# Performance work log

Hardware: AMD Instinct MI355X
Metric: run time of the kernel (lower is better)

## Reference

```python
import jax, jax.numpy as jnp
import numpy as np

TWO_PI = 2.0 * np.pi


def _fftfreq(n, d):
    # numpy-compatible fftfreq, trace/grad-safe in d: [0..n/2-1, -n/2..-1]/(n*d)
    k = jnp.arange(n)
    k = jnp.where(k < (n + 1) // 2, k, k - n).astype(jnp.float32)
    return k / (n * d)


def _forward(x, wp1_re, wp1_im, wp2_re, wp2_im, wr_re, wr_im, ty, tx):
    wp1 = (wp1_re + 1j * wp1_im).astype(jnp.complex64)   # [Ci,Co,m1]
    wp2 = (wp2_re + 1j * wp2_im).astype(jnp.complex64)   # [Ci,Co,m2]
    wr = (wr_re + 1j * wr_im).astype(jnp.complex64)      # [Ci,Co,m1,m2]
    Ny, Nx = x.shape[-2], x.shape[-1]
    dty = ty[1] - ty[0]
    dtx = tx[1] - tx[0]

    alpha = jnp.fft.fft2(x, axes=(-2, -1))               # [B,Ci,Ny,Nx] complex
    lam1 = (1j * TWO_PI * _fftfreq(Ny, dty)).astype(jnp.complex64)  # [Ny]
    lam2 = (1j * TWO_PI * _fftfreq(Nx, dtx)).astype(jnp.complex64)  # [Nx]

    # Pole-residue transfer function factors: Hw = wr / ((lam1-p1)(lam2-p2))
    A1 = 1.0 / (lam1 - wp1[..., None])                   # [Ci,Co,m1,Ny]
    A2 = 1.0 / (lam2 - wp2[..., None])                   # [Ci,Co,m2,Nx]

    # sum over poles (p,q) of Hw -> [Ci,Co,Ny,Nx]
    Hsum = jnp.einsum('ikpq,ikpo,ikqx->ikox', wr, A1, A2)
    res1 = jnp.einsum('biox,ikox->bkox', alpha, Hsum)    # [B,Co,Ny,Nx]
    # sum over frequency grid (o,x) -> residue coefficients [B,Co,m1,m2]
    res2 = jnp.einsum('biox,ikpq,ikpo,ikqx->bkpq', alpha, wr, A1, A2)

    x1 = jnp.real(jnp.fft.ifft2(res1, s=(Ny, Nx), axes=(-2, -1)))

    # explicit pole-exponential evaluation over the spatial grid
    E1 = jnp.exp(wp1[..., None] * ty.astype(jnp.complex64))  # [Ci,Co,m1,Ny]
    E2 = jnp.exp(wp2[..., None] * tx.astype(jnp.complex64))  # [Ci,Co,m2,Nx]
    # res2 channel dim contracts against E1/E2's first (in==out required)
    x2 = jnp.real(jnp.einsum('kbpq,bipz,biqx->kizx', res2, E1, E2)) / (Nx * Ny)
    return x1 + x2


def setup_inputs() -> dict:
    key = jax.random.key(0)
    B, Ci, Co, Ny, Nx, m1, m2 = 8, 32, 32, 128, 128, 4, 5
    ks = jax.random.split(key, 7)
    scale = 1.0 / (Ci * Co)
    x = jax.random.normal(ks[0], (B, Ci, Ny, Nx), jnp.float32)
    wp1_re = scale * jax.random.uniform(ks[1], (Ci, Co, m1), jnp.float32)
    wp1_im = scale * jax.random.uniform(ks[2], (Ci, Co, m1), jnp.float32)
    wp2_re = scale * jax.random.uniform(ks[3], (Ci, Co, m2), jnp.float32)
    wp2_im = scale * jax.random.uniform(ks[4], (Ci, Co, m2), jnp.float32)
    wr_re = scale * jax.random.uniform(ks[5], (Ci, Co, m1, m2), jnp.float32)
    wr_im = scale * jax.random.uniform(ks[6], (Ci, Co, m1, m2), jnp.float32)
    ty = (jnp.arange(Ny) / Ny).astype(jnp.float32)
    tx = (jnp.arange(Nx) / Nx).astype(jnp.float32)
    return dict(x=x, wp1_re=wp1_re, wp1_im=wp1_im, wp2_re=wp2_re, wp2_im=wp2_im,
                wr_re=wr_re, wr_im=wr_im, ty=ty, tx=tx)


def reference(x, wp1_re, wp1_im, wp2_re, wp2_im, wr_re, wr_im, ty, tx):
    return _forward(x, wp1_re, wp1_im, wp2_re, wp2_im, wr_re, wr_im, ty, tx)
```

## Files before the change

### kernel.cpp

```cpp
#include <hip/hip_runtime.h>
#include <math.h>

#define N 128
#define B 8
#define CI 32
#define CO 32
#define M1 4
#define M2 5
#define IK (CI*CO)
#define IKP (IK*M1)
#define IKQ (IK*M2)
#define TWO_PI_F 6.2831853071795864769f

__device__ __forceinline__ float2 cmul(float2 a, float2 b){
    return make_float2(fmaf(a.x,b.x,-(a.y*b.y)), fmaf(a.x,b.y,a.y*b.x));
}
__device__ __forceinline__ float2 cmadd(float2 acc, float2 a, float2 b){
    acc.x = fmaf(a.x, b.x, fmaf(-a.y, b.y, acc.x));
    acc.y = fmaf(a.x, b.y, fmaf( a.y, b.x, acc.y));
    return acc;
}

__global__ void k_A1T(const float* wr_, const float* wi_, const float* t_, float2* A1T){
    int idx = blockIdx.x*256 + threadIdx.x;
    int o   = idx >> 12;
    int ikp = idx & (IKP-1);
    float d = t_[1]-t_[0];
    float invnd = 1.0f/((float)N*d);
    int kk = (o < N/2) ? o : o - N;
    float lam = TWO_PI_F * (float)kk * invnd;
    float dr = -wr_[ikp];
    float di = lam - wi_[ikp];
    float inv = 1.0f/(dr*dr + di*di);
    A1T[idx] = make_float2(dr*inv, -di*inv);
}

__global__ void k_A2(const float* wr_, const float* wi_, const float* t_, float2* A2){
    int idx = blockIdx.x*256 + threadIdx.x;
    int ikq = idx >> 7; int xx = idx & (N-1);
    float d = t_[1]-t_[0];
    float invnd = 1.0f/((float)N*d);
    int kk = (xx < N/2) ? xx : xx - N;
    float lam = TWO_PI_F * (float)kk * invnd;
    float dr = -wr_[ikq];
    float di = lam - wi_[ikq];
    float inv = 1.0f/(dr*dr + di*di);
    A2[idx] = make_float2(dr*inv, -di*inv);
}

__global__ void k_E(const float* wr_, const float* wi_, const float* t_, float2* E){
    int idx = blockIdx.x*256 + threadIdx.x;
    int ikp = idx >> 7; int y = idx & (N-1);
    float t = t_[y];
    float m = expf(wr_[ikp]*t);
    float s, c; sincosf(wi_[ikp]*t, &s, &c);
    E[idx] = make_float2(m*c, m*s);
}

__global__ void k_W2N(const float* wrr, const float* wri, const float2* A2, float2* W2N){
    int idx = blockIdx.x*256 + threadIdx.x;
    int ikp = idx >> 7; int xx = idx & (N-1);
    int ik = ikp >> 2; int p = ikp & 3;
    float2 acc = make_float2(0.f,0.f);
    const float* wr0 = wrr + ik*(M1*M2) + p*M2;
    const float* wi0 = wri + ik*(M1*M2) + p*M2;
    const float2* a2 = A2 + (size_t)ik*(M2*N) + xx;
    #pragma unroll
    for(int q=0;q<M2;q++){
        float2 w = make_float2(wr0[q], wi0[q]);
        acc = cmadd(acc, w, a2[q*N]);
    }
    W2N[(size_t)ikp*N + xx] = acc;
}

template<int SIGNPOS, int REALIN, int SCALE>
__global__ void __launch_bounds__(256) k_fft_rows(const void* in_, float2* out){
    const float sgn = SIGNPOS ? 1.0f : -1.0f;
    __shared__ float tre[16*132];
    __shared__ float tim_[16*132];
    __shared__ float zre[16*136];
    __shared__ float zim[16*136];
    int t = threadIdx.x;
    size_t row0 = (size_t)blockIdx.x * 16;

    if(REALIN){
        const float* src = (const float*)in_ + row0*N;
        #pragma unroll
        for(int j=0;j<8;j++){
            int idx = t + 256*j; int r = idx>>7, cl = idx&127;
            tre[r*132+cl] = src[idx];
        }
    } else {
        const float2* src = (const float2*)in_ + row0*N;
        #pragma unroll
        for(int j=0;j<8;j++){
            int idx = t + 256*j; int r = idx>>7, cl = idx&127;
            float2 v = src[idx];
            tre[r*132+cl] = v.x; tim_[r*132+cl] = v.y;
        }
    }
    float t16c[16], t16s[16];
    #pragma unroll
    for(int j=0;j<16;j++){ float s,c; sincosf(sgn*(TWO_PI_F/16.f)*(float)j, &s,&c); t16c[j]=c; t16s[j]=s; }
    __syncthreads();

    int r = t>>4, u = t&15, b = u&7, h = u>>3;
    float xr[16], xi[16];
    #pragma unroll
    for(int a=0;a<16;a++){
        float vr = tre[r*132 + 8*a + b];
        float vi = REALIN ? 0.f : tim_[r*132 + 8*a + b];
        if(h && (a&1)){ vr = -vr; vi = -vi; }
        xr[a]=vr; xi[a]=vi;
    }
    #pragma unroll
    for(int cc=0; cc<8; cc++){
        float yr=0.f, yi=0.f;
        #pragma unroll
        for(int a=0;a<16;a++){
            int j = (a*cc)&15;
            if(REALIN){
                yr = fmaf(xr[a], t16c[j], yr);
                yi = fmaf(xr[a], t16s[j], yi);
            } else {
                yr = fmaf(xr[a], t16c[j], yr); yr = fmaf(-xi[a], t16s[j], yr);
                yi = fmaf(xr[a], t16s[j], yi); yi = fmaf( xi[a], t16c[j], yi);
            }
        }
        int c = 8*h + cc;
        float s,co; sincosf(sgn*(TWO_PI_F/128.f)*(float)(b*c), &s,&co);
        zre[r*136 + b*17 + c] = fmaf(yr,co,-(yi*s));
        zim[r*136 + b*17 + c] = fmaf(yr,s,  yi*co);
    }
    __syncthreads();

    float t8c[8], t8s[8];
    #pragma unroll
    for(int j=0;j<8;j++){ float s,c; sincosf(sgn*(TWO_PI_F/8.f)*(float)j, &s,&c); t8c[j]=c; t8s[j]=s; }
    int r2 = t>>4, c2 = t&15;
    float zr_[8], zi_[8];
    #pragma unroll
    for(int bb=0;bb<8;bb++){ zr_[bb]=zre[r2*136 + bb*17 + c2]; zi_[bb]=zim[r2*136 + bb*17 + c2]; }
    float2* dst = out + (row0 + r2)*N;
    #pragma unroll
    for(int d=0; d<8; d++){
        float Xr=0.f, Xi=0.f;
        #pragma unroll
        for(int bb=0;bb<8;bb++){
            int j=(bb*d)&7;
            Xr = fmaf(zr_[bb], t8c[j], Xr); Xr = fmaf(-zi_[bb], t8s[j], Xr);
            Xi = fmaf(zr_[bb], t8s[j], Xi); Xi = fmaf( zi_[bb], t8c[j], Xi);
        }
        if(SCALE){ Xr *= (1.f/128.f); Xi *= (1.f/128.f); }
        dst[c2 + 16*d] = make_float2(Xr, Xi);
    }
}

template<int SIGNPOS, int REALOUT, int SCALE>
__global__ void __launch_bounds__(256) k_fft_cols(const float2* in, float2* outc, float* outr){
    const float sgn = SIGNPOS ? 1.0f : -1.0f;
    __shared__ float tre[N*17];
    __shared__ float tim_[N*17];
    __shared__ float zre[8*16*17];
    __shared__ float zim[8*16*17];
    int t = threadIdx.x;
    int img = blockIdx.x >> 3; int x0 = (blockIdx.x & 7)*16;
    const float2* src = in + (size_t)img*N*N + x0;
    #pragma unroll
    for(int j=0;j<8;j++){
        int idx = t + 256*j; int y = idx>>4, xc = idx&15;
        float2 v = src[y*N + xc];
        tre[y*17+xc]=v.x; tim_[y*17+xc]=v.y;
    }
    float t16c[16], t16s[16];
    #pragma unroll
    for(int j=0;j<16;j++){ float s,c; sincosf(sgn*(TWO_PI_F/16.f)*(float)j, &s,&c); t16c[j]=c; t16s[j]=s; }
    __syncthreads();

    int xc = t&15, u = t>>4, b = u&7, h = u>>3;
    float xr[16], xi[16];
    #pragma unroll
    for(int a=0;a<16;a++){
        int y = 8*a + b;
        float vr = tre[y*17+xc];
        float vi = tim_[y*17+xc];
        if(h && (a&1)){ vr = -vr; vi = -vi; }
        xr[a]=vr; xi[a]=vi;
    }
    #pragma unroll
    for(int cc=0; cc<8; cc++){
        float yr=0.f, yi=0.f;
        #pragma unroll
        for(int a=0;a<16;a++){
            int j = (a*cc)&15;
            yr = fmaf(xr[a], t16c[j], yr); yr = fmaf(-xi[a], t16s[j], yr);
            yi = fmaf(xr[a], t16s[j], yi); yi = fmaf( xi[a], t16c[j], yi);
        }
        int c = 8*h + cc;
        float s,co; sincosf(sgn*(TWO_PI_F/128.f)*(float)(b*c), &s,&co);
        zre[(b*16 + c)*17 + xc] = fmaf(yr,co,-(yi*s));
        zim[(b*16 + c)*17 + xc] = fmaf(yr,s,  yi*co);
    }
    __syncthreads();

    float t8c[8], t8s[8];
    #pragma unroll
    for(int j=0;j<8;j++){ float s,c; sincosf(sgn*(TWO_PI_F/8.f)*(float)j, &s,&c); t8c[j]=c; t8s[j]=s; }
    int c2 = t>>4; int x2 = t&15;
    float zr_[8], zi_[8];
    #pragma unroll
    for(int bb=0;bb<8;bb++){ zr_[bb]=zre[(bb*16 + c2)*17 + x2]; zi_[bb]=zim[(bb*16 + c2)*17 + x2]; }
    #pragma unroll
    for(int d=0; d<8; d++){
        float Xr=0.f, Xi=0.f;
        #pragma unroll
        for(int bb=0;bb<8;bb++){
            int j=(bb*d)&7;
            Xr = fmaf(zr_[bb], t8c[j], Xr); Xr = fmaf(-zi_[bb], t8s[j], Xr);
            Xi = fmaf(zr_[bb], t8s[j], Xi); Xi = fmaf( zi_[bb], t8c[j], Xi);
        }
        int ky = c2 + 16*d;
        if(REALOUT){
            outr[(size_t)img*N*N + ky*N + x0 + x2] = Xr * (SCALE ? (1.f/128.f) : 1.f);
        } else {
            if(SCALE){ Xr *= (1.f/128.f); Xi *= (1.f/128.f); }
            outc[(size_t)img*N*N + ky*N + x0 + x2] = make_float2(Xr, Xi);
        }
    }
}

__global__ void __launch_bounds__(256) k_res1(const float2* alpha, const float2* A1T,
                                              const float2* W2N, float2* res1){
    __shared__ float4 At4[B*CI*8];
    int t = threadIdx.x;
    int o  = blockIdx.x >> 3;
    int x0 = (blockIdx.x & 7) * 16;

    {
        int im0 = t >> 3, xq = t & 7;
        #pragma unroll
        for(int j=0;j<8;j++){
            int im = im0 + 32*j;
            At4[im*8 + xq] = *(const float4*)(alpha + (size_t)im*(N*N) + o*N + x0 + 2*xq);
        }
    }
    __syncthreads();

    int k = t >> 3, xh = t & 7;
    float2 acc[B][2];
    #pragma unroll
    for(int b=0;b<B;b++){ acc[b][0]=make_float2(0.f,0.f); acc[b][1]=make_float2(0.f,0.f); }

    const float2* a1base = A1T + (size_t)o*IKP + k*M1;
    const float2* w2base = W2N + ((size_t)k*M1)*N + x0 + 2*xh;

    #pragma unroll 2
    for(int i=0;i<CI;i++){
        float4 a1a = *(const float4*)(a1base + (size_t)i*128);
        float4 a1b = *(const float4*)(a1base + (size_t)i*128 + 2);
        float2 a1v[M1] = { make_float2(a1a.x,a1a.y), make_float2(a1a.z,a1a.w),
                           make_float2(a1b.x,a1b.y), make_float2(a1b.z,a1b.w) };
        float2 h0 = make_float2(0.f,0.f), h1 = make_float2(0.f,0.f);
        const float2* w2 = w2base + (size_t)i*(128*N);
        #pragma unroll
        for(int p=0;p<M1;p++){
            float4 wv = *(const float4*)(w2 + (size_t)p*N);
            h0 = cmadd(h0, a1v[p], make_float2(wv.x,wv.y));
            h1 = cmadd(h1, a1v[p], make_float2(wv.z,wv.w));
        }
        #pragma unroll
        for(int b=0;b<B;b++){
            float4 av = At4[(b*CI + i)*8 + xh];
            acc[b][0] = cmadd(acc[b][0], make_float2(av.x,av.y), h0);
            acc[b][1] = cmadd(acc[b][1], make_float2(av.z,av.w), h1);
        }
    }

    #pragma unroll
    for(int b=0;b<B;b++){
        float4 v = make_float4(acc[b][0].x, acc[b][0].y, acc[b][1].x, acc[b][1].y);
        *(float4*)(res1 + (size_t)(b*CO + k)*(N*N) + o*N + x0 + 2*xh) = v;
    }
}

__global__ void __launch_bounds__(512, 4) k_S_res2(const float2* alpha, const float2* A2,
                                                   const float2* A1T, float2* part){
    __shared__ float2 tile[64*33];
    __shared__ float2 A2c[160*33];
    int t = threadIdx.x;
    int ol = t & 15;
    int kl = t >> 4;
    int bid = blockIdx.x;
    int oh = bid & 1;
    int i  = (bid >> 1) & (CI-1);
    int b  = bid >> 6;
    int ik = i*CO + kl;
    const float2* asrc = alpha + ((size_t)(b*CI + i))*(N*N) + (size_t)oh*64*N;
    const float2* a2base = A2 + (size_t)i*(CO*M2*N);

    const int txc = t & 31, trow = t >> 5;
    float2 U[4][5];
    #pragma unroll
    for(int oi=0;oi<4;oi++)
        #pragma unroll
        for(int q=0;q<5;q++) U[oi][q] = make_float2(0.f,0.f);

    float2 pre[4];
    #pragma unroll
    for(int j=0;j<4;j++) pre[j] = asrc[(trow + 16*j)*N + txc];

    for(int c=0; c<4; c++){
        __syncthreads();
        #pragma unroll
        for(int j=0;j<4;j++) tile[(trow + 16*j)*33 + txc] = pre[j];
        #pragma unroll
        for(int s=0;s<10;s++){
            int rs = s*16 + trow;
            A2c[rs*33 + txc] = a2base[(size_t)rs*N + c*32 + txc];
        }
        if(c < 3){
            #pragma unroll
            for(int j=0;j<4;j++) pre[j] = asrc[(trow + 16*j)*N + (c+1)*32 + txc];
        }
        __syncthreads();
        #pragma unroll 4
        for(int xc=0; xc<32; xc++){
            float2 a2v[5];
            const float2* a2row = A2c + (kl*5)*33 + xc;
            #pragma unroll
            for(int q=0;q<5;q++) a2v[q] = a2row[q*33];
            #pragma unroll
            for(int oi=0;oi<4;oi++){
                float2 av = tile[(ol + 16*oi)*33 + xc];
                #pragma unroll
                for(int q=0;q<5;q++) U[oi][q] = cmadd(U[oi][q], av, a2v[q]);
            }
        }
    }

    float2 S[4][5];
    #pragma unroll
    for(int p=0;p<4;p++)
        #pragma unroll
        for(int q=0;q<5;q++) S[p][q] = make_float2(0.f,0.f);
    #pragma unroll
    for(int oi=0;oi<4;oi++){
        int o = oh*64 + ol + 16*oi;
        const float2* a1 = A1T + (size_t)o*IKP + (size_t)ik*M1;
        float2 a1v[4];
        #pragma unroll
        for(int p=0;p<4;p++) a1v[p] = a1[p];
        #pragma unroll
        for(int p=0;p<4;p++)
            #pragma unroll
            for(int q=0;q<5;q++) S[p][q] = cmadd(S[p][q], a1v[p], U[oi][q]);
    }
    #pragma unroll
    for(int m=1;m<16;m<<=1){
        #pragma unroll
        for(int p=0;p<4;p++)
            #pragma unroll
            for(int q=0;q<5;q++){
                S[p][q].x += __shfl_xor(S[p][q].x, m);
                S[p][q].y += __shfl_xor(S[p][q].y, m);
            }
    }
    if(ol==0){
        float2* dst = part + ((size_t)((b*CO + kl)*CI + i)*2 + oh)*(M1*M2);
        #pragma unroll
        for(int p=0;p<4;p++)
            #pragma unroll
            for(int q=0;q<5;q++) dst[p*5+q] = S[p][q];
    }
}

__global__ void k_res2_red(const float2* part, const float* wrr, const float* wri, float2* res2){
    int bk = blockIdx.x;
    int t = threadIdx.x;
    int i = t & 31, g = t >> 5;
    int k = bk & (CO-1);
    int ikk = i*CO + k;
    float2 acc[5];
    #pragma unroll
    for(int e=0;e<5;e++){
        int pq = g*5 + e;
        float2 w = make_float2(wrr[ikk*(M1*M2)+pq], wri[ikk*(M1*M2)+pq]);
        const float2* pp = part + ((size_t)(bk*CI + i)*2)*(M1*M2) + pq;
        float2 s0 = pp[0], s1 = pp[M1*M2];
        float2 s = make_float2(s0.x+s1.x, s0.y+s1.y);
        acc[e] = cmul(w, s);
    }
    #pragma unroll
    for(int m=1;m<32;m<<=1){
        #pragma unroll
        for(int e=0;e<5;e++){
            acc[e].x += __shfl_xor(acc[e].x, m);
            acc[e].y += __shfl_xor(acc[e].y, m);
        }
    }
    if(i==0){
        #pragma unroll
        for(int e=0;e<5;e++) res2[(size_t)bk*(M1*M2) + g*5 + e] = acc[e];
    }
}

__global__ void __launch_bounds__(256) k_x2(const float2* res2, const float2* E1,
                                            const float2* E2, float* out){
    __shared__ __align__(16) float2 res2s[CI*M1*M2];
    __shared__ __align__(16) float2 Wt[M1*N];
    __shared__ __align__(16) float2 buf[2][M1*64 + M2*N];
    int t = threadIdx.x;
    int yh = blockIdx.x & 1;
    int j  = (blockIdx.x >> 1) & (CO-1);
    int b  = blockIdx.x >> 6;
    int xt = t & 15, yt = t >> 4;

    {
        const float4* s4 = (const float4*)(res2 + (size_t)b*CO*M1*M2);
        float4* d4 = (float4*)res2s;
        d4[t] = s4[t];
        if(t < 64) d4[256+t] = s4[256+t];
    }

    const bool is1_0 = (t < 128);
    const bool ok1 = (t < 192);
    int off0, dst0;
    if(is1_0){ int pp = t >> 5, rem = (t & 31) << 1; off0 = pp*N + rem; dst0 = pp*64 + rem; }
    else     { int g = t - 128; int qq = g >> 6, xi = (g & 63) << 1; off0 = qq*N + xi; dst0 = 256 + qq*128 + xi; }
    int g1 = t + 128; int qq1 = g1 >> 6, xi1 = (g1 & 63) << 1;
    int off1 = qq1*N + xi1;
    int dst1 = 256 + qq1*128 + xi1;

    const float2* E1c = E1 + ((size_t)j*M1)*N + yh*64;
    const float2* E2c = E2 + ((size_t)j*M2)*N;

    float4 pre0 = *(const float4*)((is1_0 ? E1c : E2c) + off0);
    float4 pre1 = ok1 ? *(const float4*)(E2c + off1) : make_float4(0.f,0.f,0.f,0.f);
    *(float4*)(&buf[0][dst0]) = pre0;
    if(ok1) *(float4*)(&buf[0][dst1]) = pre1;
    int cur = 0;
    __syncthreads();

    float acc[4][8];
    #pragma unroll
    for(int yy=0;yy<4;yy++)
        #pragma unroll
        for(int s=0;s<8;s++) acc[yy][s] = 0.f;

    for(int c=0; c<CI; c++){
        const float2* E2s = buf[cur] + 256;
        #pragma unroll
        for(int s=0;s<2;s++){
            int e = t + 256*s;
            int pp = e >> 7, xi = e & 127;
            const float2* rr = res2s + c*(M1*M2) + pp*M2;
            float2 w = make_float2(0.f,0.f);
            #pragma unroll
            for(int q=0;q<M2;q++) w = cmadd(w, rr[q], E2s[q*128 + xi]);
            Wt[pp*128 + xi] = w;
        }
        if(c+1 < CI){
            E1c += (size_t)CO*M1*N;
            E2c += (size_t)CO*M2*N;
            pre0 = *(const float4*)((is1_0 ? E1c : E2c) + off0);
            if(ok1) pre1 = *(const float4*)(E2c + off1);
        }
        __syncthreads();

        const float2* E1s = buf[cur];
        #pragma unroll
        for(int p=0;p<4;p++){
            float2 e1[4];
            float4 a  = *(const float4*)(E1s + p*64 + yt*4);
            float4 bq = *(const float4*)(E1s + p*64 + yt*4 + 2);
            e1[0]=make_float2(a.x,a.y);  e1[1]=make_float2(a.z,a.w);
            e1[2]=make_float2(bq.x,bq.y); e1[3]=make_float2(bq.z,bq.w);
            #pragma unroll
            for(int s=0;s<4;s++){
                float4 wv = *(const float4*)(Wt + p*128 + 32*s + 2*xt);
                #pragma unroll
                for(int yy=0;yy<4;yy++){
                    float2 e = e1[yy];
                    acc[yy][2*s]   = fmaf(e.x, wv.x, fmaf(-e.y, wv.y, acc[yy][2*s]));
                    acc[yy][2*s+1] = fmaf(e.x, wv.z, fmaf(-e.y, wv.w, acc[yy][2*s+1]));
                }
            }
        }
        if(c+1 < CI){
            float2* nb = buf[cur^1];
            *(float4*)(nb + dst0) = pre0;
            if(ok1) *(float4*)(nb + dst1) = pre1;
        }
        cur ^= 1;
        __syncthreads();
    }

    const float sc = 1.0f/((float)N*(float)N);
    size_t base = (size_t)(b*CO + j)*(N*N) + (size_t)yh*64*N;
    #pragma unroll
    for(int yy=0;yy<4;yy++){
        float* orow = out + base + (size_t)(yt*4 + yy)*N;
        #pragma unroll
        for(int s=0;s<4;s++){
            float2* dst = (float2*)(orow + 32*s + 2*xt);
            float2 old = *dst;
            *dst = make_float2(old.x + acc[yy][2*s]*sc, old.y + acc[yy][2*s+1]*sc);
        }
    }
}

extern "C" void kernel_launch(void* const* d_in, const int* in_sizes, int n_in,
                              void* d_out, int out_size, void* d_ws, size_t ws_size,
                              hipStream_t stream){
    const float* x    = (const float*)d_in[0];
    const float* wp1r = (const float*)d_in[1];
    const float* wp1i = (const float*)d_in[2];
    const float* wp2r = (const float*)d_in[3];
    const float* wp2i = (const float*)d_in[4];
    const float* wrr  = (const float*)d_in[5];
    const float* wri  = (const float*)d_in[6];
    const float* ty   = (const float*)d_in[7];
    const float* tx   = (const float*)d_in[8];
    float* out = (float*)d_out;
    float2* ws = (float2*)d_ws;

    const size_t NCIMG = (size_t)B*CI*N*N;
    float2* bufA  = ws;
    float2* alpha = bufA  + NCIMG;
    float2* res1  = alpha + NCIMG;
    float2* A1T   = res1  + NCIMG;
    float2* A2    = A1T   + (size_t)N*IKP;
    float2* W2N   = A2    + (size_t)IKQ*N;
    float2* E1    = W2N   + (size_t)N*IKP;
    float2* E2    = E1    + (size_t)IKP*N;
    float2* res2  = E2    + (size_t)IKQ*N;
    float2* part  = res2  + (size_t)B*CO*M1*M2;

    k_A1T<<<(N*IKP)/256, 256, 0, stream>>>(wp1r, wp1i, ty, A1T);
    k_E  <<<(IKP*N)/256, 256, 0, stream>>>(wp1r, wp1i, ty, E1);
    k_A2 <<<(IKQ*N)/256, 256, 0, stream>>>(wp2r, wp2i, tx, A2);
    k_E  <<<(IKQ*N)/256, 256, 0, stream>>>(wp2r, wp2i, tx, E2);
    k_W2N<<<(IKP*N)/256, 256, 0, stream>>>(wrr, wri, A2, W2N);

    k_fft_rows<0,1,0><<<(B*CI*N)/16, 256, 0, stream>>>((const void*)x, bufA);
    k_fft_cols<0,0,0><<<B*CI*8, 256, 0, stream>>>(bufA, alpha, nullptr);

    k_res1<<<N*8, 256, 0, stream>>>(alpha, A1T, W2N, res1);
    k_S_res2<<<B*CI*2, 512, 0, stream>>>(alpha, A2, A1T, part);
    k_res2_red<<<B*CO, 128, 0, stream>>>(part, wrr, wri, res2);

    k_fft_rows<1,0,1><<<(B*CO*N)/16, 256, 0, stream>>>((const void*)res1, bufA);
    k_fft_cols<1,1,1><<<B*CO*8, 256, 0, stream>>>(bufA, nullptr, out);
    k_x2<<<B*CO*2, 256, 0, stream>>>(res2, E1, E2, out);
}
```

Measured before the change: 310.4 us.

## Share FFT twiddles via LDS table and split x2 kernel into quarter-row blocks

Both FFT kernels now build a 128-entry sin/cos table in shared memory once per block and read all radix-16, radix-8 and inter-stage twiddles from it, replacing per-thread sincosf calls. Separately, the x2 kernel tiles the output in quarters of rows instead of halves, doubling the grid with two rows per thread and a smaller E1 staging buffer. This targets transcendental ALU cost in the FFTs and low occupancy in x2. The trade-off is recomputing the Wt contraction twice as often across blocks, plus extra LDS reads.

Result: no change. 309.8 us (-0.2%).

```diff
diff --git a/kernel.cpp b/kernel.cpp
--- a/kernel.cpp
+++ b/kernel.cpp
@@ -80,8 +80,11 @@
     __shared__ float tim_[16*132];
     __shared__ float zre[16*136];
     __shared__ float zim[16*136];
+    __shared__ float twc[128], tws[128];
     int t = threadIdx.x;
     size_t row0 = (size_t)blockIdx.x * 16;
+
+    if(t < 128){ float s,c; sincosf(sgn*(TWO_PI_F/128.f)*(float)t, &s,&c); twc[t]=c; tws[t]=s; }
 
     if(REALIN){
         const float* src = (const float*)in_ + row0*N;
@@ -99,10 +102,11 @@
             tre[r*132+cl] = v.x; tim_[r*132+cl] = v.y;
         }
     }
+    __syncthreads();
+
     float t16c[16], t16s[16];
     #pragma unroll
-    for(int j=0;j<16;j++){ float s,c; sincosf(sgn*(TWO_PI_F/16.f)*(float)j, &s,&c); t16c[j]=c; t16s[j]=s; }
-    __syncthreads();
+    for(int j=0;j<16;j++){ t16c[j]=twc[8*j]; t16s[j]=tws[8*j]; }
 
     int r = t>>4, u = t&15, b = u&7, h = u>>3;
     float xr[16], xi[16];
@@ -128,7 +132,8 @@
             }
         }
         int c = 8*h + cc;
-        float s,co; sincosf(sgn*(TWO_PI_F/128.f)*(float)(b*c), &s,&co);
+        int jw = b*c;
+        float co = twc[jw], s = tws[jw];
         zre[r*136 + b*17 + c] = fmaf(yr,co,-(yi*s));
         zim[r*136 + b*17 + c] = fmaf(yr,s,  yi*co);
     }
@@ -136,7 +141,7 @@
 
     float t8c[8], t8s[8];
     #pragma unroll
-    for(int j=0;j<8;j++){ float s,c; sincosf(sgn*(TWO_PI_F/8.f)*(float)j, &s,&c); t8c[j]=c; t8s[j]=s; }
+    for(int j=0;j<8;j++){ t8c[j]=twc[16*j]; t8s[j]=tws[16*j]; }
     int r2 = t>>4, c2 = t&15;
     float zr_[8], zi_[8];
     #pragma unroll
@@ -163,8 +168,12 @@
     __shared__ float tim_[N*17];
     __shared__ float zre[8*16*17];
     __shared__ float zim[8*16*17];
+    __shared__ float twc[128], tws[128];
     int t = threadIdx.x;
     int img = blockIdx.x >> 3; int x0 = (blockIdx.x & 7)*16;
+
+    if(t < 128){ float s,c; sincosf(sgn*(TWO_PI_F/128.f)*(float)t, &s,&c); twc[t]=c; tws[t]=s; }
+
     const float2* src = in + (size_t)img*N*N + x0;
     #pragma unroll
     for(int j=0;j<8;j++){
@@ -172,10 +181,11 @@
         float2 v = src[y*N + xc];
         tre[y*17+xc]=v.x; tim_[y*17+xc]=v.y;
     }
+    __syncthreads();
+
     float t16c[16], t16s[16];
     #pragma unroll
-    for(int j=0;j<16;j++){ float s,c; sincosf(sgn*(TWO_PI_F/16.f)*(float)j, &s,&c); t16c[j]=c; t16s[j]=s; }
-    __syncthreads();
+    for(int j=0;j<16;j++){ t16c[j]=twc[8*j]; t16s[j]=tws[8*j]; }
 
     int xc = t&15, u = t>>4, b = u&7, h = u>>3;
     float xr[16], xi[16];
@@ -197,7 +207,8 @@
             yi = fmaf(xr[a], t16s[j], yi); yi = fmaf( xi[a], t16c[j], yi);
         }
         int c = 8*h + cc;
-        float s,co; sincosf(sgn*(TWO_PI_F/128.f)*(float)(b*c), &s,&co);
+        int jw = b*c;
+        float co = twc[jw], s = tws[jw];
         zre[(b*16 + c)*17 + xc] = fmaf(yr,co,-(yi*s));
         zim[(b*16 + c)*17 + xc] = fmaf(yr,s,  yi*co);
     }
@@ -205,7 +216,7 @@
 
     float t8c[8], t8s[8];
     #pragma unroll
-    for(int j=0;j<8;j++){ float s,c; sincosf(sgn*(TWO_PI_F/8.f)*(float)j, &s,&c); t8c[j]=c; t8s[j]=s; }
+    for(int j=0;j<8;j++){ t8c[j]=twc[16*j]; t8s[j]=tws[16*j]; }
     int c2 = t>>4; int x2 = t&15;
     float zr_[8], zi_[8];
     #pragma unroll
@@ -408,11 +419,11 @@
                                             const float2* E2, float* out){
     __shared__ __align__(16) float2 res2s[CI*M1*M2];
     __shared__ __align__(16) float2 Wt[M1*N];
-    __shared__ __align__(16) float2 buf[2][M1*64 + M2*N];
+    __shared__ __align__(16) float2 buf[2][M1*32 + M2*N];
     int t = threadIdx.x;
-    int yh = blockIdx.x & 1;
-    int j  = (blockIdx.x >> 1) & (CO-1);
-    int b  = blockIdx.x >> 6;
+    int yq = blockIdx.x & 3;
+    int j  = (blockIdx.x >> 2) & (CO-1);
+    int b  = blockIdx.x >> 7;
     int xt = t & 15, yt = t >> 4;
 
     {
@@ -422,16 +433,16 @@
         if(t < 64) d4[256+t] = s4[256+t];
     }
 
-    const bool is1_0 = (t < 128);
-    const bool ok1 = (t < 192);
+    const bool is1_0 = (t < 64);
+    const bool ok1 = (t < 128);
     int off0, dst0;
-    if(is1_0){ int pp = t >> 5, rem = (t & 31) << 1; off0 = pp*N + rem; dst0 = pp*64 + rem; }
-    else     { int g = t - 128; int qq = g >> 6, xi = (g & 63) << 1; off0 = qq*N + xi; dst0 = 256 + qq*128 + xi; }
-    int g1 = t + 128; int qq1 = g1 >> 6, xi1 = (g1 & 63) << 1;
+    if(is1_0){ int pp = t >> 4, rem = (t & 15) << 1; off0 = pp*N + rem; dst0 = pp*32 + rem; }
+    else     { int g = t - 64; int qq = g >> 6, xi = (g & 63) << 1; off0 = qq*N + xi; dst0 = 128 + qq*128 + xi; }
+    int g1 = t + 192; int qq1 = g1 >> 6, xi1 = (g1 & 63) << 1;
     int off1 = qq1*N + xi1;
-    int dst1 = 256 + qq1*128 + xi1;
-
-    const float2* E1c = E1 + ((size_t)j*M1)*N + yh*64;
+    int dst1 = 128 + qq1*128 + xi1;
+
+    const float2* E1c = E1 + ((size_t)j*M1)*N + yq*32;
     const float2* E2c = E2 + ((size_t)j*M2)*N;
 
     float4 pre0 = *(const float4*)((is1_0 ? E1c : E2c) + off0);
@@ -441,14 +452,14 @@
     int cur = 0;
     __syncthreads();
 
-    float acc[4][8];
-    #pragma unroll
-    for(int yy=0;yy<4;yy++)
+    float acc[2][8];
+    #pragma unroll
+    for(int yy=0;yy<2;yy++)
         #pragma unroll
         for(int s=0;s<8;s++) acc[yy][s] = 0.f;
 
     for(int c=0; c<CI; c++){
-        const float2* E2s = buf[cur] + 256;
+        const float2* E2s = buf[cur] + 128;
         #pragma unroll
         for(int s=0;s<2;s++){
             int e = t + 256*s;
@@ -470,20 +481,16 @@
         const float2* E1s = buf[cur];
         #pragma unroll
         for(int p=0;p<4;p++){
-            float2 e1[4];
-            float4 a  = *(const float4*)(E1s + p*64 + yt*4);
-            float4 bq = *(const float4*)(E1s + p*64 + yt*4 + 2);
-            e1[0]=make_float2(a.x,a.y);  e1[1]=make_float2(a.z,a.w);
-            e1[2]=make_float2(bq.x,bq.y); e1[3]=make_float2(bq.z,bq.w);
+            float4 a = *(const float4*)(E1s + p*32 + yt*2);
+            float2 e0 = make_float2(a.x,a.y);
+            float2 e1v = make_float2(a.z,a.w);
             #pragma unroll
             for(int s=0;s<4;s++){
                 float4 wv = *(const float4*)(Wt + p*128 + 32*s + 2*xt);
-                #pragma unroll
-                for(int yy=0;yy<4;yy++){
-                    float2 e = e1[yy];
-                    acc[yy][2*s]   = fmaf(e.x, wv.x, fmaf(-e.y, wv.y, acc[yy][2*s]));
-                    acc[yy][2*s+1] = fmaf(e.x, wv.z, fmaf(-e.y, wv.w, acc[yy][2*s+1]));
-                }
+                acc[0][2*s]   = fmaf(e0.x, wv.x, fmaf(-e0.y, wv.y, acc[0][2*s]));
+                acc[0][2*s+1] = fmaf(e0.x, wv.z, fmaf(-e0.y, wv.w, acc[0][2*s+1]));
+                acc[1][2*s]   = fmaf(e1v.x, wv.x, fmaf(-e1v.y, wv.y, acc[1][2*s]));
+                acc[1][2*s+1] = fmaf(e1v.x, wv.z, fmaf(-e1v.y, wv.w, acc[1][2*s+1]));
             }
         }
         if(c+1 < CI){
@@ -496,10 +503,10 @@
     }
 
     const float sc = 1.0f/((float)N*(float)N);
-    size_t base = (size_t)(b*CO + j)*(N*N) + (size_t)yh*64*N;
-    #pragma unroll
-    for(int yy=0;yy<4;yy++){
-        float* orow = out + base + (size_t)(yt*4 + yy)*N;
+    size_t base = (size_t)(b*CO + j)*(N*N) + (size_t)(yq*32)*N;
+    #pragma unroll
+    for(int yy=0;yy<2;yy++){
+        float* orow = out + base + (size_t)(yt*2 + yy)*N;
         #pragma unroll
         for(int s=0;s<4;s++){
             float2* dst = (float2*)(orow + 32*s + 2*xt);
@@ -551,5 +558,5 @@
 
     k_fft_rows<1,0,1><<<(B*CO*N)/16, 256, 0, stream>>>((const void*)res1, bufA);
     k_fft_cols<1,1,1><<<B*CO*8, 256, 0, stream>>>(bufA, nullptr, out);
-    k_x2<<<B*CO*2, 256, 0, stream>>>(res2, E1, E2, out);
-}
+    k_x2<<<B*CO*4, 256, 0, stream>>>(res2, E1, E2, out);
+}
```
